# Optimization experiments

Hardware: AMD Instinct MI355X
Metric: run time of the kernel (lower is better)

Reference implementation:

```python
import jax, jax.numpy as jnp
import numpy as np

N_ATOMS = 51200
N_MOL = 512
FEAT = 384


def setup_inputs() -> dict:
    key = jax.random.key(0)
    ks = jax.random.split(key, 20)
    s = 0.05  # small random weights instead of the degenerate zero-init
    inp = {
        "node_feats": jax.random.normal(ks[0], (N_ATOMS, FEAT), jnp.float32),
        "energy": jax.random.normal(ks[1], (N_MOL,), jnp.float32),
        "forces": jax.random.normal(ks[2], (N_ATOMS, 3), jnp.float32),
        "stress": jax.random.normal(ks[3], (N_MOL, 3, 3), jnp.float32),
        "W1": jax.random.normal(ks[4], (64, 256), jnp.float32) * s,
        "b1": jnp.zeros((64,), jnp.float32),
        "W2": jax.random.normal(ks[5], (16, 64), jnp.float32) * s,
        "b2": jnp.zeros((16,), jnp.float32),
        "W3": jax.random.normal(ks[6], (1, 16), jnp.float32) * s,
        "b3": jnp.zeros((1,), jnp.float32),
        "W1f": jax.random.normal(ks[7], (64, 256), jnp.float32) * s,
        "b1f": jnp.zeros((64,), jnp.float32),
        "W2f": jax.random.normal(ks[8], (16, 64), jnp.float32) * s,
        "b2f": jnp.zeros((16,), jnp.float32),
        "W3f": jax.random.normal(ks[9], (1, 16), jnp.float32) * s,
        "b3f": jnp.zeros((1,), jnp.float32),
        "S_uncert": jnp.zeros((1,), jnp.float32),
        # atom -> molecule segment ids (sorted, every molecule non-empty)
        "batch_idx": jnp.repeat(jnp.arange(N_MOL, dtype=jnp.int64), N_ATOMS // N_MOL),
    }
    return inp


def _mlp(x, W1, b1, W2, b2, W3, b3):
    h = jax.nn.silu(x @ W1.T + b1)
    h = jax.nn.silu(h @ W2.T + b2)
    return h @ W3.T + b3  # [N, 1]


def reference(node_feats, energy, forces, stress,
              W1, b1, W2, b2, W3, b3,
              W1f, b1f, W2f, b2f, W3f, b3f,
              S_uncert, batch_idx):
    # concat first 128 and last 128 feature channels -> [N, 256]
    nf = jnp.concatenate([node_feats[:, :128], node_feats[:, -128:]], axis=1)

    # E head: faithfully zeroed out and replaced by constant 0.6
    e_stds = jnp.exp(_mlp(nf, W1, b1, W2, b2, W3, b3))[:, 0] * 0 + 0.6  # [N]
    # F head
    f_u = jnp.exp(_mlp(nf, W1f, b1f, W2f, b2f, W3f, b3f))[:, 0] * 0.1   # [N]
    force_uncert = jnp.stack([f_u, f_u, f_u], axis=-1)                  # [N, 3]
    # stress uncert: constant 0.1/16 (S_uncert term zeroed, kept faithfully)
    stress_uncert = jnp.ones_like(stress) * jnp.exp(S_uncert[0]) * 0 + 0.1 / 16

    # per-molecule mean of e_stds via segment sums (scatter_add in torch)
    eu_sum = jax.ops.segment_sum(e_stds, batch_idx, num_segments=N_MOL)
    n_atoms = jax.ops.segment_sum(jnp.ones_like(e_stds), batch_idx, num_segments=N_MOL)
    energy_uncert = eu_sum / n_atoms  # [n_mol]

    return (energy, forces, stress, energy_uncert, force_uncert, stress_uncert)
```

## Files before the change

### kernel.cpp

```cpp
#include <hip/hip_runtime.h>
#include <hip/hip_bf16.h>

#define N_ATOMS 51200

#define OUT_FUNC 159232

typedef __attribute__((ext_vector_type(4))) float f32x4;
typedef __attribute__((ext_vector_type(4))) unsigned u32x4;
typedef __attribute__((ext_vector_type(8))) short s16x8;

constexpr int BLK = 256;

__device__ __forceinline__ unsigned pack2(float lo, float hi) {
    return __builtin_amdgcn_perm(__float_as_uint(hi), __float_as_uint(lo), 0x07060302);
}
__device__ __forceinline__ s16x8 pack8(f32x4 lo, f32x4 hi) {
    union { u32x4 u; s16x8 s; } c;
    c.u.x = pack2(lo.x, lo.y); c.u.y = pack2(lo.z, lo.w);
    c.u.z = pack2(hi.x, hi.y); c.u.w = pack2(hi.z, hi.w);
    return c.s;
}
__device__ __forceinline__ short bftrunc(float x) {
    return (short)(__float_as_uint(x) >> 16);
}
__device__ __forceinline__ float silu_(float v) { return v / (1.0f + __expf(-v)); }

__global__ __launch_bounds__(BLK, 4) void funcert_kernel(
    const float* __restrict__ nf,
    const float* __restrict__ energy,
    const float* __restrict__ forces,
    const float* __restrict__ stress,
    const float* __restrict__ W1f, const float* __restrict__ b1f,
    const float* __restrict__ W2f, const float* __restrict__ b2f,
    const float* __restrict__ W3f, const float* __restrict__ b3f,
    float* __restrict__ out)
{
    const int t   = threadIdx.x;
    const int gid = blockIdx.x * BLK + t;

    __shared__ float Xq[2][64 * 64];
    __shared__ short H1s[64 * 64];

    const int lane  = t & 63;
    const int w     = t >> 6;
    const int g     = lane >> 4;
    const int col   = lane & 15;
    const int abase = blockIdx.x * 64;
    const int ch    = w * 16 + col;

    const int rloc = lane >> 4;
    const int sl   = lane & 15;

    #define GLD_Q(b, qf)                                                     \
        { _Pragma("unroll")                                                  \
          for (int i2 = 0; i2 < 4; ++i2) {                                   \
              const int ii = w * 4 + i2;                                     \
              const int r  = 4 * ii + rloc;                                  \
              const int c  = sl ^ ((r & 7) << 1);                            \
              const float* src = nf + (size_t)(abase + r) * 384 + (qf) + c * 4; \
              __builtin_amdgcn_global_load_lds(                              \
                  (const __attribute__((address_space(1))) void*)src,        \
                  (__attribute__((address_space(3))) void*)(&Xq[b][ii * 256]), \
                  16, 0, 0);                                                 \
          } }

    #define WQ_ISSUE(dst, q)                                                 \
        { _Pragma("unroll")                                                  \
          for (int ks2 = 0; ks2 < 2; ++ks2) {                                \
              const float* p = W1f + ch * 256 + (q) * 64 + ks2 * 32 + g * 8; \
              dst[2 * ks2]     = *(const f32x4*)p;                           \
              dst[2 * ks2 + 1] = *(const f32x4*)(p + 4);                     \
          } }

    #define Q_COMPUTE(b, wfv)                                                \
        { _Pragma("unroll")                                                  \
          for (int mt = 0; mt < 4; ++mt) {                                   \
              const int row = mt * 16 + col;                                 \
              const int xr  = (row & 7) << 1;                                \
              _Pragma("unroll")                                              \
              for (int ks2 = 0; ks2 < 2; ++ks2) {                            \
                  const int s0 = ((ks2 << 3) + (g << 1)) ^ xr;               \
                  const float* p = &Xq[b][row * 64 + s0 * 4];                \
                  const f32x4 lo = *(const f32x4*)p;                         \
                  const f32x4 hi = *(const f32x4*)(p + 4);                   \
                  acc[mt] = __builtin_amdgcn_mfma_f32_16x16x32_bf16(         \
                              pack8(lo, hi), wfv[ks2], acc[mt], 0, 0, 0);    \
              } } }

    f32x4 cv = {0.f, 0.f, 0.f, 0.f}; int co = -1;
    if (gid < 40960) {
        co = gid;
        if      (gid < 128)   { cv = ((const f32x4*)energy)[gid]; }
        else if (gid < 38528) { cv = ((const f32x4*)forces)[gid - 128]; }
        else if (gid < 39680) { cv = ((const f32x4*)stress)[gid - 38528]; }
        else if (gid < 39808) { cv = (f32x4){0.6f, 0.6f, 0.6f, 0.6f}; }
        else { cv = (f32x4){0.00625f, 0.00625f, 0.00625f, 0.00625f}; co = gid + 38400; }
    }

    f32x4 wv[4];
    WQ_ISSUE(wv, 0);
    const float b1v = b1f[ch];
    GLD_Q(0, 0);

    s16x8 wf[2];
    wf[0] = pack8(wv[0], wv[1]); wf[1] = pack8(wv[2], wv[3]);

    f32x4 acc[4];
    #pragma unroll
    for (int mt = 0; mt < 4; ++mt) acc[mt] = (f32x4){0.f, 0.f, 0.f, 0.f};

    __syncthreads();
    WQ_ISSUE(wv, 1);
    GLD_Q(1, 64);
    Q_COMPUTE(0, wf);
    __syncthreads();

    wf[0] = pack8(wv[0], wv[1]); wf[1] = pack8(wv[2], wv[3]);
    WQ_ISSUE(wv, 2);
    GLD_Q(0, 256);
    Q_COMPUTE(1, wf);
    __syncthreads();

    wf[0] = pack8(wv[0], wv[1]); wf[1] = pack8(wv[2], wv[3]);
    WQ_ISSUE(wv, 3);
    GLD_Q(1, 320);
    Q_COMPUTE(0, wf);
    __syncthreads();

    wf[0] = pack8(wv[0], wv[1]); wf[1] = pack8(wv[2], wv[3]);
    Q_COMPUTE(1, wf);

    #pragma unroll
    for (int mt = 0; mt < 4; ++mt) {
        #pragma unroll
        for (int r = 0; r < 4; ++r) {
            const int atom = mt * 16 + g * 4 + r;
            H1s[atom * 64 + ch] = bftrunc(silu_(acc[mt][r] + b1v));
        }
    }
    __syncthreads();

    s16x8 w2frag[2];
    #pragma unroll
    for (int ks = 0; ks < 2; ++ks) {
        const float* p = W2f + col * 64 + ks * 32 + g * 8;
        w2frag[ks] = pack8(*(const f32x4*)p, *(const f32x4*)(p + 4));
    }
    const int arow = w * 16 + col;
    f32x4 a2 = {0.f, 0.f, 0.f, 0.f};
    #pragma unroll
    for (int ks = 0; ks < 2; ++ks) {
        const s16x8 af = *(const s16x8*)(H1s + arow * 64 + ks * 32 + g * 8);
        a2 = __builtin_amdgcn_mfma_f32_16x16x32_bf16(af, w2frag[ks], a2, 0, 0, 0);
    }

    const float b2v = b2f[col];
    const float w3v = W3f[col];
    float y[4];
    #pragma unroll
    for (int r = 0; r < 4; ++r)
        y[r] = silu_(a2[r] + b2v) * w3v;
    #pragma unroll
    for (int m = 1; m < 16; m <<= 1) {
        #pragma unroll
        for (int r = 0; r < 4; ++r)
            y[r] += __shfl_xor(y[r], m, 64);
    }
    const float b3v = b3f[0];
    float fu[4];
    #pragma unroll
    for (int r = 0; r < 4; ++r)
        fu[r] = __expf(y[r] + b3v) * 0.1f;

    if (col < 12) {
        const int a_ = col / 3, c = col - a_ * 3;
        const float v = (a_ == 0) ? fu[0] : (a_ == 1) ? fu[1] : (a_ == 2) ? fu[2] : fu[3];
        const int atom = w * 16 + g * 4 + a_;
        out[OUT_FUNC + 3 * (abase + atom) + c] = v;
    }

    if (co >= 0) ((f32x4*)out)[co] = cv;
}

extern "C" void kernel_launch(void* const* d_in, const int* in_sizes, int n_in,
                              void* d_out, int out_size, void* d_ws, size_t ws_size,
                              hipStream_t stream) {
    const float* nf     = (const float*)d_in[0];
    const float* energy = (const float*)d_in[1];
    const float* forces = (const float*)d_in[2];
    const float* stress = (const float*)d_in[3];
    const float* W1f    = (const float*)d_in[10];
    const float* b1f    = (const float*)d_in[11];
    const float* W2f    = (const float*)d_in[12];
    const float* b2f    = (const float*)d_in[13];
    const float* W3f    = (const float*)d_in[14];
    const float* b3f    = (const float*)d_in[15];
    float* out = (float*)d_out;

    dim3 grid(N_ATOMS / 64);
    funcert_kernel<<<grid, BLK, 0, stream>>>(nf, energy, forces, stress,
                                             W1f, b1f, W2f, b2f, W3f, b3f, out);
}
```

Before: 21.30 us.

## Deepen prefetch pipeline with explicit vmcnt waits instead of full syncthreads

Issues the first two quarter-tiles of node features and weights up front, using two register weight buffers. The full __syncthreads calls are replaced by partial s_waitcnt vmcnt(8) plus raw s_barrier, so one tile's loads stay in flight while the previous tile computes. The aim is to hide global load latency behind the MFMA work. It relies on hand-counted outstanding load counts, and a miscount or compiler reordering of loads could give races or wrong results.

Result: no change. 21.04 us (-1.2%).

```diff
diff --git a/kernel.cpp b/kernel.cpp
--- a/kernel.cpp
+++ b/kernel.cpp
@@ -24,6 +24,11 @@
     return (short)(__float_as_uint(x) >> 16);
 }
 __device__ __forceinline__ float silu_(float v) { return v / (1.0f + __expf(-v)); }
+
+#define VMCNT8()  asm volatile("s_waitcnt vmcnt(8)" ::: "memory")
+#define VMCNT0()  asm volatile("s_waitcnt vmcnt(0)" ::: "memory")
+#define LGKM0()   asm volatile("s_waitcnt lgkmcnt(0)" ::: "memory")
+#define RAWBAR()  asm volatile("s_barrier" ::: "memory")
 
 __global__ __launch_bounds__(BLK, 4) void funcert_kernel(
     const float* __restrict__ nf,
@@ -97,37 +102,38 @@
         else { cv = (f32x4){0.00625f, 0.00625f, 0.00625f, 0.00625f}; co = gid + 38400; }
     }
 
-    f32x4 wv[4];
-    WQ_ISSUE(wv, 0);
+    f32x4 wva[4], wvb[4];
+    WQ_ISSUE(wva, 0);
+    GLD_Q(0, 0);
+    WQ_ISSUE(wvb, 1);
+    GLD_Q(1, 64);
     const float b1v = b1f[ch];
-    GLD_Q(0, 0);
-
+
+    f32x4 acc[4];
+    #pragma unroll
+    for (int mt = 0; mt < 4; ++mt) acc[mt] = (f32x4){0.f, 0.f, 0.f, 0.f};
     s16x8 wf[2];
-    wf[0] = pack8(wv[0], wv[1]); wf[1] = pack8(wv[2], wv[3]);
-
-    f32x4 acc[4];
-    #pragma unroll
-    for (int mt = 0; mt < 4; ++mt) acc[mt] = (f32x4){0.f, 0.f, 0.f, 0.f};
-
-    __syncthreads();
-    WQ_ISSUE(wv, 1);
-    GLD_Q(1, 64);
+
+    VMCNT8(); RAWBAR();
+    wf[0] = pack8(wva[0], wva[1]); wf[1] = pack8(wva[2], wva[3]);
     Q_COMPUTE(0, wf);
-    __syncthreads();
-
-    wf[0] = pack8(wv[0], wv[1]); wf[1] = pack8(wv[2], wv[3]);
-    WQ_ISSUE(wv, 2);
+    LGKM0(); RAWBAR();
+    WQ_ISSUE(wva, 2);
     GLD_Q(0, 256);
+
+    VMCNT8(); RAWBAR();
+    wf[0] = pack8(wvb[0], wvb[1]); wf[1] = pack8(wvb[2], wvb[3]);
     Q_COMPUTE(1, wf);
-    __syncthreads();
-
-    wf[0] = pack8(wv[0], wv[1]); wf[1] = pack8(wv[2], wv[3]);
-    WQ_ISSUE(wv, 3);
+    LGKM0(); RAWBAR();
+    WQ_ISSUE(wvb, 3);
     GLD_Q(1, 320);
+
+    VMCNT8(); RAWBAR();
+    wf[0] = pack8(wva[0], wva[1]); wf[1] = pack8(wva[2], wva[3]);
     Q_COMPUTE(0, wf);
-    __syncthreads();
-
-    wf[0] = pack8(wv[0], wv[1]); wf[1] = pack8(wv[2], wv[3]);
+
+    VMCNT0(); RAWBAR();
+    wf[0] = pack8(wvb[0], wvb[1]); wf[1] = pack8(wvb[2], wvb[3]);
     Q_COMPUTE(1, wf);
 
     #pragma unroll
```

## Switch layer-1 staging to triple-buffered 32-column chunks with raw vmcnt barriers

Applied to the files above, without the earlier changes.

Replaces the double-buffered 64-column feature staging with eight 32-column chunks in a three-slot LDS ring. Loads are issued two stages ahead and synchronised with explicit s_waitcnt vmcnt plus raw s_barrier instead of __syncthreads, so more memory traffic stays in flight while the MFMAs run. The swizzle changes to match the 32-float rows, and launch bounds rise to 5 blocks per CU now that LDS use is smaller. The risks are hand-counted vmcnt values (weight loads share the counter), more barriers overall, and register pressure from three weight buffers.

After: 19.90 us. -6.6%, faster.

```diff
diff --git a/kernel.cpp b/kernel.cpp
--- a/kernel.cpp
+++ b/kernel.cpp
@@ -25,7 +25,11 @@
 }
 __device__ __forceinline__ float silu_(float v) { return v / (1.0f + __expf(-v)); }
 
-__global__ __launch_bounds__(BLK, 4) void funcert_kernel(
+#define VMCNT4()  asm volatile("s_waitcnt vmcnt(4)" ::: "memory")
+#define VMCNT0()  asm volatile("s_waitcnt vmcnt(0)" ::: "memory")
+#define RAWBAR()  asm volatile("s_barrier" ::: "memory")
+
+__global__ __launch_bounds__(BLK, 5) void funcert_kernel(
     const float* __restrict__ nf,
     const float* __restrict__ energy,
     const float* __restrict__ forces,
@@ -38,7 +42,7 @@
     const int t   = threadIdx.x;
     const int gid = blockIdx.x * BLK + t;
 
-    __shared__ float Xq[2][64 * 64];
+    __shared__ float Xe[3][64 * 32];
     __shared__ short H1s[64 * 64];
 
     const int lane  = t & 63;
@@ -48,44 +52,38 @@
     const int abase = blockIdx.x * 64;
     const int ch    = w * 16 + col;
 
-    const int rloc = lane >> 4;
-    const int sl   = lane & 15;
+    const int rloc = lane >> 3;
+    const int sl   = lane & 7;
 
-    #define GLD_Q(b, qf)                                                     \
+    #define GLD_E(buf, e)                                                    \
         { _Pragma("unroll")                                                  \
-          for (int i2 = 0; i2 < 4; ++i2) {                                   \
-              const int ii = w * 4 + i2;                                     \
-              const int r  = 4 * ii + rloc;                                  \
-              const int c  = sl ^ ((r & 7) << 1);                            \
-              const float* src = nf + (size_t)(abase + r) * 384 + (qf) + c * 4; \
+          for (int i = 0; i < 2; ++i) {                                      \
+              const int br = w * 16 + i * 8;                                 \
+              const float* src = nf + (size_t)(abase + br + rloc) * 384      \
+                                 + (32 * (e) + ((e) >= 4 ? 128 : 0))         \
+                                 + ((sl ^ rloc) << 2);                       \
               __builtin_amdgcn_global_load_lds(                              \
                   (const __attribute__((address_space(1))) void*)src,        \
-                  (__attribute__((address_space(3))) void*)(&Xq[b][ii * 256]), \
+                  (__attribute__((address_space(3))) void*)((buf) + br * 32),\
                   16, 0, 0);                                                 \
           } }
 
-    #define WQ_ISSUE(dst, q)                                                 \
-        { _Pragma("unroll")                                                  \
-          for (int ks2 = 0; ks2 < 2; ++ks2) {                                \
-              const float* p = W1f + ch * 256 + (q) * 64 + ks2 * 32 + g * 8; \
-              dst[2 * ks2]     = *(const f32x4*)p;                           \
-              dst[2 * ks2 + 1] = *(const f32x4*)(p + 4);                     \
-          } }
+    #define WQ_E(dst, e)                                                     \
+        { const float* p = W1f + ch * 256 + (e) * 32 + g * 8;                \
+          dst[0] = *(const f32x4*)p;                                         \
+          dst[1] = *(const f32x4*)(p + 4); }
 
-    #define Q_COMPUTE(b, wfv)                                                \
-        { _Pragma("unroll")                                                  \
+    #define COMP_E(buf, wvv)                                                 \
+        { const s16x8 wf = pack8(wvv[0], wvv[1]);                            \
+          _Pragma("unroll")                                                  \
           for (int mt = 0; mt < 4; ++mt) {                                   \
               const int row = mt * 16 + col;                                 \
-              const int xr  = (row & 7) << 1;                                \
-              _Pragma("unroll")                                              \
-              for (int ks2 = 0; ks2 < 2; ++ks2) {                            \
-                  const int s0 = ((ks2 << 3) + (g << 1)) ^ xr;               \
-                  const float* p = &Xq[b][row * 64 + s0 * 4];                \
-                  const f32x4 lo = *(const f32x4*)p;                         \
-                  const f32x4 hi = *(const f32x4*)(p + 4);                   \
-                  acc[mt] = __builtin_amdgcn_mfma_f32_16x16x32_bf16(         \
-                              pack8(lo, hi), wfv[ks2], acc[mt], 0, 0, 0);    \
-              } } }
+              const int s0  = (2 * g) ^ (row & 7);                           \
+              const f32x4 lo = *(const f32x4*)((buf) + row * 32 + (s0)      * 4); \
+              const f32x4 hi = *(const f32x4*)((buf) + row * 32 + (s0 ^ 1)  * 4); \
+              acc[mt] = __builtin_amdgcn_mfma_f32_16x16x32_bf16(             \
+                          pack8(lo, hi), wf, acc[mt], 0, 0, 0);              \
+          } }
 
     f32x4 cv = {0.f, 0.f, 0.f, 0.f}; int co = -1;
     if (gid < 40960) {
@@ -97,38 +95,23 @@
         else { cv = (f32x4){0.00625f, 0.00625f, 0.00625f, 0.00625f}; co = gid + 38400; }
     }
 
-    f32x4 wv[4];
-    WQ_ISSUE(wv, 0);
     const float b1v = b1f[ch];
-    GLD_Q(0, 0);
-
-    s16x8 wf[2];
-    wf[0] = pack8(wv[0], wv[1]); wf[1] = pack8(wv[2], wv[3]);
+    f32x4 wvA[2], wvB[2], wvC[2];
+    GLD_E(Xe[0], 0);  WQ_E(wvA, 0);
+    GLD_E(Xe[1], 1);  WQ_E(wvB, 1);
 
     f32x4 acc[4];
     #pragma unroll
     for (int mt = 0; mt < 4; ++mt) acc[mt] = (f32x4){0.f, 0.f, 0.f, 0.f};
 
-    __syncthreads();
-    WQ_ISSUE(wv, 1);
-    GLD_Q(1, 64);
-    Q_COMPUTE(0, wf);
-    __syncthreads();
-
-    wf[0] = pack8(wv[0], wv[1]); wf[1] = pack8(wv[2], wv[3]);
-    WQ_ISSUE(wv, 2);
-    GLD_Q(0, 256);
-    Q_COMPUTE(1, wf);
-    __syncthreads();
-
-    wf[0] = pack8(wv[0], wv[1]); wf[1] = pack8(wv[2], wv[3]);
-    WQ_ISSUE(wv, 3);
-    GLD_Q(1, 320);
-    Q_COMPUTE(0, wf);
-    __syncthreads();
-
-    wf[0] = pack8(wv[0], wv[1]); wf[1] = pack8(wv[2], wv[3]);
-    Q_COMPUTE(1, wf);
+    VMCNT4(); RAWBAR();  GLD_E(Xe[2], 2); WQ_E(wvC, 2);  COMP_E(Xe[0], wvA);
+    VMCNT4(); RAWBAR();  GLD_E(Xe[0], 3); WQ_E(wvA, 3);  COMP_E(Xe[1], wvB);
+    VMCNT4(); RAWBAR();  GLD_E(Xe[1], 4); WQ_E(wvB, 4);  COMP_E(Xe[2], wvC);
+    VMCNT4(); RAWBAR();  GLD_E(Xe[2], 5); WQ_E(wvC, 5);  COMP_E(Xe[0], wvA);
+    VMCNT4(); RAWBAR();  GLD_E(Xe[0], 6); WQ_E(wvA, 6);  COMP_E(Xe[1], wvB);
+    VMCNT4(); RAWBAR();  GLD_E(Xe[1], 7); WQ_E(wvB, 7);  COMP_E(Xe[2], wvC);
+    VMCNT4(); RAWBAR();                                  COMP_E(Xe[0], wvA);
+    VMCNT0(); RAWBAR();                                  COMP_E(Xe[1], wvB);
 
     #pragma unroll
     for (int mt = 0; mt < 4; ++mt) {
```
